# Kernel optimization log

Measured on AMD Instinct MI355X. Metric: run time of the kernel, lower is better.

## Reference

```python
import jax, jax.numpy as jnp
import numpy as np

N_NODES = 100000
N_EDGES = 1600000
N_GRAPHS = 128
D = 128          # input_dim == hidden_dim
OUT = 64         # output_dim (num classes)
L = 4            # num_layers - 1 GIN message-passing layers
BN_EPS = 1e-5


def setup_inputs() -> dict:
    key = jax.random.key(0)
    ks = jax.random.split(key, 12)
    s = 1.0 / np.sqrt(D)
    x = jax.random.normal(ks[0], (N_NODES, D), jnp.float32)
    edge_src = jax.random.randint(ks[1], (N_GRAPHS * 0 + N_EDGES,), 0, N_NODES, jnp.int32)
    edge_dst = jax.random.randint(ks[2], (N_EDGES,), 0, N_NODES, jnp.int32)
    graph_ids = jnp.sort(jax.random.randint(ks[3], (N_NODES,), 0, N_GRAPHS, jnp.int32))
    return {
        'x': x,
        'edge_src': edge_src,
        'edge_dst': edge_dst,
        'graph_ids': graph_ids,
        'eps': jnp.zeros((L,), jnp.float32),
        'W1': jax.random.normal(ks[4], (L, D, D), jnp.float32) * s,
        'b1': jnp.zeros((L, D), jnp.float32),
        'g1': jnp.ones((L, D), jnp.float32),
        'be1': jnp.zeros((L, D), jnp.float32),
        'W2': jax.random.normal(ks[5], (L, D, D), jnp.float32) * s,
        'b2': jnp.zeros((L, D), jnp.float32),
        'g2': jnp.ones((L, D), jnp.float32),
        'be2': jnp.zeros((L, D), jnp.float32),
        'predW': jax.random.normal(ks[6], (L + 1, D, OUT), jnp.float32) * s,
        'predb': jnp.zeros((L + 1, OUT), jnp.float32),
    }


def _bn(h, g, b):
    # BatchNorm1d in training mode: batch mean / biased variance over nodes
    mu = jnp.mean(h, axis=0)
    var = jnp.var(h, axis=0)
    return g * (h - mu) * jax.lax.rsqrt(var + BN_EPS) + b


def reference(x, edge_src, edge_dst, graph_ids, eps, W1, b1, g1, be1,
              W2, b2, g2, be2, predW, predb):
    n = x.shape[0]
    hidden = [x]
    h = x
    for l in range(L):
        # sparse Adj @ h : gather neighbor feats at edges, scatter-add to dst
        agg = jax.ops.segment_sum(h[edge_src], edge_dst, num_segments=n)
        pooled = agg + (1.0 + eps[l]) * h                      # GIN eps update
        z = jax.nn.relu(_bn(pooled @ W1[l] + b1[l], g1[l], be1[l]))  # MLP hidden
        z = z @ W2[l] + b2[l]                                  # MLP out
        h = jax.nn.relu(_bn(z, g2[l], be2[l]))                 # outer BN + relu
        hidden.append(h)
    # GIN readout: sum graph pooling + per-layer linear prediction (dropout p=0)
    score = jnp.zeros((N_GRAPHS, OUT), jnp.float32)
    for l, hl in enumerate(hidden):
        pooled_g = jax.ops.segment_sum(hl, graph_ids, num_segments=N_GRAPHS)
        score = score + pooled_g @ predW[l] + predb[l]
    return score
```

## Files before the change

### kernel.cpp

```cpp
#include <hip/hip_runtime.h>

#define NN 100000
#define NE 1600000
#define NG 128
#define DIM 128
#define OUTD 64
#define NL 4
#define SLCAP 48
#define NBKT 391
#define BCAP 6144
#define ECH 4096
#define EBLKS ((NE + ECH - 1) / ECH)
#define NPB 128
#define YSTR 136

typedef __attribute__((ext_vector_type(8))) short bf16x8;
typedef __attribute__((ext_vector_type(4))) float floatx4;
typedef __attribute__((ext_vector_type(2))) float floatx2;

__device__ __forceinline__ float bf_lo(unsigned u) {
    union { unsigned u; float f; } c; c.u = u << 16; return c.f;
}
__device__ __forceinline__ float bf_hi(unsigned u) {
    union { unsigned u; float f; } c; c.u = u & 0xffff0000u; return c.f;
}
__device__ __forceinline__ unsigned f2bf(float x) {
    union { float f; unsigned u; } c; c.f = x;
    return (c.u + 0x7fffu + ((c.u >> 16) & 1u)) >> 16;
}
__device__ __forceinline__ float bfs2f(short s) {
    union { unsigned u; float f; } c; c.u = ((unsigned)(unsigned short)s) << 16; return c.f;
}

__device__ __forceinline__ void bn_coef(const float* __restrict__ stat,
                                        const float* __restrict__ gamma,
                                        const float* __restrict__ beta,
                                        int f, float& a, float& c) {
    float mu = stat[f] * (1.0f / NN);
    float var = fmaf(-mu, mu, stat[DIM + f] * (1.0f / NN));
    a = gamma[f] * rsqrtf(var + 1e-5f);
    c = fmaf(-mu, a, beta[f]);
}

__global__ __launch_bounds__(256)
void bucketize(const int* __restrict__ esrc, const int* __restrict__ edst,
               int* __restrict__ gcnt, unsigned* __restrict__ bkt) {
    __shared__ int lh[NBKT];
    for (int b = threadIdx.x; b < NBKT; b += 256) lh[b] = 0;
    __syncthreads();
    const int e0 = blockIdx.x * ECH;
    const int e1 = min(e0 + ECH, NE);
    for (int e = e0 + threadIdx.x; e < e1; e += 256)
        atomicAdd(&lh[(unsigned)edst[e] >> 8], 1);
    __syncthreads();
    for (int b = threadIdx.x; b < NBKT; b += 256) {
        int c = lh[b];
        lh[b] = (c > 0) ? atomicAdd(&gcnt[b], c) : 0;
    }
    __syncthreads();
    for (int e = e0 + threadIdx.x; e < e1; e += 256) {
        unsigned d = (unsigned)edst[e];
        unsigned b = d >> 8;
        int p = atomicAdd(&lh[b], 1);
        if (p < BCAP)
            bkt[(size_t)b * BCAP + p] = (unsigned)esrc[e] | ((d & 255u) << 24);
    }
}

__global__ __launch_bounds__(256)
void bucket_to_slots(const unsigned* __restrict__ bkt, const int* __restrict__ gcnt,
                     int* __restrict__ cnt, int* __restrict__ slot) {
    __shared__ int lslot[256 * SLCAP];
    __shared__ int lc[256];
    const int b = blockIdx.x, t = threadIdx.x;
    lc[t] = 0;
    __syncthreads();
    int ne = gcnt[b]; if (ne > BCAP) ne = BCAP;
    const unsigned* be = bkt + (size_t)b * BCAP;
    for (int i = t; i < ne; i += 256) {
        unsigned v = be[i];
        int local = v >> 24;
        int pos = atomicAdd(&lc[local], 1);
        if (pos < SLCAP) lslot[local * SLCAP + pos] = (int)(v & 0xFFFFFFu);
    }
    __syncthreads();
    const int node = b * 256 + t;
    if (node < NN) cnt[node] = min(lc[t], SLCAP);
    const size_t base = (size_t)b * (256 * SLCAP);
    for (int i = t; i < 256 * SLCAP; i += 256)
        slot[base + i] = lslot[i];
}

__global__ void to_bf16(const float* __restrict__ x, unsigned* __restrict__ xb) {
    size_t i = ((size_t)blockIdx.x * 256 + threadIdx.x) * 4;
    float4 v = *(const float4*)(x + i);
    uint2 o;
    o.x = f2bf(v.x) | (f2bf(v.y) << 16);
    o.y = f2bf(v.z) | (f2bf(v.w) << 16);
    *(uint2*)(xb + i / 2) = o;
}

__global__ void build_wt(const float* __restrict__ W1, const float* __restrict__ W2,
                         unsigned short* __restrict__ Wt) {
    int b = blockIdx.x;
    const float* W = ((b & 1) ? W2 : W1) + (size_t)(b >> 1) * DIM * DIM;
    unsigned short* O = Wt + (size_t)b * DIM * DIM;
    int i = blockIdx.y * 2048 + threadIdx.x;
    for (int j = 0; j < 8; ++j, i += 256) {
        int k = i >> 7, n = i & 127;
        O[n * DIM + k] = (unsigned short)f2bf(W[i]);
    }
}

__global__ void csr_agg(const unsigned* __restrict__ hq, const int* __restrict__ cnt,
                        const int* __restrict__ slot, const float* __restrict__ eps, int l,
                        unsigned* __restrict__ outq) {
    const int t = threadIdx.x;
    const int node = blockIdx.x * 4 + (t >> 6);
    const int lane = t & 63;
    const int chunk = lane & 15;
    const int grp = lane >> 4;
    const uint4* __restrict__ h4 = (const uint4*)hq;

    const int deg = cnt[node];

    floatx2 acc[4];
    {
        uint4 sv = h4[(size_t)node * 16 + chunk];
        float e1 = (grp == 0) ? (1.0f + eps[l]) : 0.0f;
        const unsigned* p = (const unsigned*)&sv;
#pragma unroll
        for (int q = 0; q < 4; ++q) {
            floatx2 v; v.x = bf_lo(p[q]); v.y = bf_hi(p[q]);
            acc[q] = e1 * v;
        }
    }

    if (deg > 0) {
        const int iters = (deg + 15) >> 4;
        const int base = node * SLCAP;
        const int hi = base + deg - 1;
        const int j0 = base + grp;
        int idx[4];
#pragma unroll
        for (int q = 0; q < 4; ++q) {
            int j = j0 + q * 4;
            int v = slot[min(j, hi)];
            idx[q] = (j <= hi) ? v : NN;
        }

        for (int it = 0; it < iters; ++it) {
            uint4 u[4];
#pragma unroll
            for (int q = 0; q < 4; ++q) u[q] = h4[(size_t)idx[q] * 16 + chunk];

            if (it + 1 < iters) {
                const int jn = j0 + (it + 1) * 16;
#pragma unroll
                for (int q = 0; q < 4; ++q) {
                    int j = jn + q * 4;
                    int v = slot[min(j, hi)];
                    idx[q] = (j <= hi) ? v : NN;
                }
            }

#pragma unroll
            for (int q = 0; q < 4; ++q) {
                const unsigned* p = (const unsigned*)&u[q];
#pragma unroll
                for (int r = 0; r < 4; ++r) {
                    floatx2 v; v.x = bf_lo(p[r]); v.y = bf_hi(p[r]);
                    acc[r] += v;
                }
            }
        }
    }

#pragma unroll
    for (int r = 0; r < 4; ++r) {
        acc[r].x += __shfl_xor(acc[r].x, 16);
        acc[r].y += __shfl_xor(acc[r].y, 16);
        acc[r].x += __shfl_xor(acc[r].x, 32);
        acc[r].y += __shfl_xor(acc[r].y, 32);
    }
    if (grp == 0) {
        uint4 o;
        unsigned* po = (unsigned*)&o;
#pragma unroll
        for (int r = 0; r < 4; ++r)
            po[r] = f2bf(acc[r].x) | (f2bf(acc[r].y) << 16);
        ((uint4*)outq)[(size_t)node * 16 + chunk] = o;
    }
}

template<int TR>
__global__ __launch_bounds__(256, 2)
void gemm_mfma(const unsigned short* __restrict__ X, const unsigned short* __restrict__ Wt,
               const float* __restrict__ bias,
               const float* __restrict__ stat, const float* __restrict__ gamma,
               const float* __restrict__ beta,
               unsigned short* __restrict__ Y, float* __restrict__ ostat) {
    __shared__ unsigned short Ws[DIM * DIM];
    __shared__ unsigned short Ys[128 * YSTR];
    __shared__ float tatc[2 * DIM];
    float* red = (float*)Ws;
    const int t = threadIdx.x;
    const int w = t >> 6, lane = t & 63;
    const int quad = lane >> 4, m = lane & 15;
    const int rowb0 = blockIdx.x * 256 + w * 32;

#pragma unroll
    for (int i = 0; i < 8; ++i) {
        int chunk = t + i * 256;
        int r = chunk >> 4, c = chunk & 15;
        ((uint4*)Ws)[(r << 4) | (c ^ (r & 15))] = ((const uint4*)Wt)[chunk];
    }
    if (TR && t < DIM) {
        float a, c;
        bn_coef(stat, gamma, beta, t, a, c);
        tatc[t] = a; tatc[DIM + t] = c;
    }

    bf16x8 a[2][4];
#pragma unroll
    for (int rt = 0; rt < 2; ++rt) {
        int row = rowb0 + rt * 16 + m;
        if (row > NN - 1) row = NN - 1;
        const unsigned short* xr = X + (size_t)row * DIM + quad * 8;
#pragma unroll
        for (int ks = 0; ks < 4; ++ks)
            a[rt][ks] = *(const bf16x8*)(xr + ks * 32);
    }
    __syncthreads();

    float sv[8], qv[8];
#pragma unroll
    for (int ct = 0; ct < 8; ++ct) { sv[ct] = 0.f; qv[ct] = 0.f; }

    for (int sub = 0; sub < 2; ++sub) {
        if (TR) {
#pragma unroll
            for (int rt = 0; rt < 2; ++rt)
#pragma unroll
                for (int ks = 0; ks < 4; ++ks) {
                    int kk = ks * 32 + quad * 8;
                    bf16x8 v = a[rt][ks];
#pragma unroll
                    for (int j = 0; j < 8; ++j) {
                        float fv = bfs2f(v[j]);
                        fv = fmaxf(fmaf(fv, tatc[kk + j], tatc[DIM + kk + j]), 0.f);
                        v[j] = (short)f2bf(fv);
                    }
                    a[rt][ks] = v;
                }
        }

        floatx4 acc[2][8];
#pragma unroll
        for (int rt = 0; rt < 2; ++rt)
#pragma unroll
            for (int ct = 0; ct < 8; ++ct) acc[rt][ct] = (floatx4)0.f;

#pragma unroll
        for (int ct = 0; ct < 8; ++ct) {
            const int row = ct * 16 + m;
            const bf16x8* wrow = (const bf16x8*)&Ws[row * DIM];
#pragma unroll
            for (int ks = 0; ks < 4; ++ks) {
                bf16x8 b = wrow[(ks * 4 + quad) ^ m];
                acc[0][ct] = __builtin_amdgcn_mfma_f32_16x16x32_bf16(a[0][ks], b, acc[0][ct], 0, 0, 0);
                acc[1][ct] = __builtin_amdgcn_mfma_f32_16x16x32_bf16(a[1][ks], b, acc[1][ct], 0, 0, 0);
            }
        }

        if (sub == 0) {
#pragma unroll
            for (int rt = 0; rt < 2; ++rt) {
                int row = rowb0 + 128 + rt * 16 + m;
                if (row > NN - 1) row = NN - 1;
                const unsigned short* xr = X + (size_t)row * DIM + quad * 8;
#pragma unroll
                for (int ks = 0; ks < 4; ++ks)
                    a[rt][ks] = *(const bf16x8*)(xr + ks * 32);
            }
        }

#pragma unroll
        for (int ct = 0; ct < 8; ++ct) {
            int col = ct * 16 + m;
            float bv = bias[col];
            float s = 0.f, q = 0.f;
#pragma unroll
            for (int rt = 0; rt < 2; ++rt) {
#pragma unroll
                for (int r = 0; r < 4; ++r) {
                    int lrow = w * 32 + rt * 16 + quad * 4 + r;
                    int row = blockIdx.x * 256 + sub * 128 + lrow;
                    float val = acc[rt][ct][r] + bv;
                    Ys[lrow * YSTR + col] = (unsigned short)f2bf(val);
                    if (row < NN) { s += val; q = fmaf(val, val, q); }
                }
            }
            sv[ct] += s; qv[ct] += q;
        }
        __syncthreads();
        {
            int lrow = t >> 1, half = t & 1;
            int grow = blockIdx.x * 256 + sub * 128 + lrow;
            if (grow < NN) {
                const uint4* srcp = (const uint4*)&Ys[lrow * YSTR + half * 64];
                uint4* dstp = (uint4*)&Y[(size_t)grow * DIM + half * 64];
#pragma unroll
                for (int i2 = 0; i2 < 8; ++i2) dstp[i2] = srcp[i2];
            }
        }
        __syncthreads();
    }

#pragma unroll
    for (int ct = 0; ct < 8; ++ct) {
        sv[ct] += __shfl_xor(sv[ct], 16); sv[ct] += __shfl_xor(sv[ct], 32);
        qv[ct] += __shfl_xor(qv[ct], 16); qv[ct] += __shfl_xor(qv[ct], 32);
    }
    __syncthreads();
#pragma unroll
    for (int ct = 0; ct < 8; ++ct) {
        int col = ct * 16 + m;
        if (quad == 0) { red[w * 256 + col] = sv[ct]; red[w * 256 + 128 + col] = qv[ct]; }
    }
    __syncthreads();
    if (t < 256) {
        float tot = red[t] + red[256 + t] + red[512 + t] + red[768 + t];
        unsafeAtomicAdd(&ostat[t], tot);
    }
}

template<int TR>
__global__ void pool_nodes(const unsigned* __restrict__ hq, const int* __restrict__ gid,
                           const float* __restrict__ stat, const float* __restrict__ gamma,
                           const float* __restrict__ beta, float* __restrict__ pg) {
    const int lane = threadIdx.x;
    int start = blockIdx.x * NPB;
    int end = start + NPB;
    if (end > NN) end = NN;
    int f = lane * 2;
    float a0 = 0.f, c0 = 0.f, a1 = 0.f, c1 = 0.f;
    if (TR) {
        bn_coef(stat, gamma, beta, f, a0, c0);
        bn_coef(stat, gamma, beta, f + 1, a1, c1);
    }
    int cur = gid[start];
    float acc0 = 0.f, acc1 = 0.f;
    for (int i0 = start; i0 < end; i0 += 4) {
        int4 g4 = *(const int4*)(gid + i0);
        unsigned uu[4];
#pragma unroll
        for (int k = 0; k < 4; ++k) uu[k] = hq[(size_t)(i0 + k) * 64 + lane];
        int gg[4] = {g4.x, g4.y, g4.z, g4.w};
#pragma unroll
        for (int k = 0; k < 4; ++k) {
            if (gg[k] != cur) {
                unsafeAtomicAdd(&pg[cur * DIM + f], acc0);
                unsafeAtomicAdd(&pg[cur * DIM + f + 1], acc1);
                acc0 = 0.f; acc1 = 0.f;
                cur = gg[k];
            }
            float x0 = bf_lo(uu[k]), x1 = bf_hi(uu[k]);
            if (TR) {
                x0 = fmaxf(fmaf(x0, a0, c0), 0.f);
                x1 = fmaxf(fmaf(x1, a1, c1), 0.f);
            }
            acc0 += x0; acc1 += x1;
        }
    }
    unsafeAtomicAdd(&pg[cur * DIM + f], acc0);
    unsafeAtomicAdd(&pg[cur * DIM + f + 1], acc1);
}

template<int WRITE>
__global__ void norm_pool(const unsigned* __restrict__ hq, const int* __restrict__ gid,
                          const float* __restrict__ stat, const float* __restrict__ gamma,
                          const float* __restrict__ beta,
                          unsigned* __restrict__ outq, float* __restrict__ pg) {
    const int lane = threadIdx.x;
    int start = blockIdx.x * NPB;
    int end = start + NPB;
    if (end > NN) end = NN;
    int f = lane * 2;
    float a0, c0, a1, c1;
    bn_coef(stat, gamma, beta, f, a0, c0);
    bn_coef(stat, gamma, beta, f + 1, a1, c1);
    int cur = gid[start];
    float acc0 = 0.f, acc1 = 0.f;
    for (int i0 = start; i0 < end; i0 += 4) {
        int4 g4 = *(const int4*)(gid + i0);
        unsigned uu[4];
#pragma unroll
        for (int k = 0; k < 4; ++k) uu[k] = hq[(size_t)(i0 + k) * 64 + lane];
        int gg[4] = {g4.x, g4.y, g4.z, g4.w};
#pragma unroll
        for (int k = 0; k < 4; ++k) {
            if (gg[k] != cur) {
                unsafeAtomicAdd(&pg[cur * DIM + f], acc0);
                unsafeAtomicAdd(&pg[cur * DIM + f + 1], acc1);
                acc0 = 0.f; acc1 = 0.f;
                cur = gg[k];
            }
            float x0 = fmaxf(fmaf(bf_lo(uu[k]), a0, c0), 0.f);
            float x1 = fmaxf(fmaf(bf_hi(uu[k]), a1, c1), 0.f);
            if (WRITE)
                outq[(size_t)(i0 + k) * 64 + lane] = f2bf(x0) | (f2bf(x1) << 16);
            acc0 += x0; acc1 += x1;
        }
    }
    unsafeAtomicAdd(&pg[cur * DIM + f], acc0);
    unsafeAtomicAdd(&pg[cur * DIM + f + 1], acc1);
}

__global__ void final_score(const float* __restrict__ pg, const float* __restrict__ predW,
                            const float* __restrict__ predb, float* __restrict__ out) {
    int g = blockIdx.x;
    int o = threadIdx.x;
    float acc = 0.f;
    for (int l = 0; l <= NL; ++l) {
        acc += predb[l * OUTD + o];
        const float* pgr = pg + ((size_t)l * NG + g) * DIM;
        const float* w = predW + (size_t)l * DIM * OUTD;
#pragma unroll 8
        for (int k = 0; k < DIM; ++k)
            acc = fmaf(pgr[k], w[k * OUTD + o], acc);
    }
    out[g * OUTD + o] = acc;
}

extern "C" void kernel_launch(void* const* d_in, const int* in_sizes, int n_in,
                              void* d_out, int out_size, void* d_ws, size_t ws_size,
                              hipStream_t stream) {
    const float* x     = (const float*)d_in[0];
    const int*   esrc  = (const int*)d_in[1];
    const int*   edst  = (const int*)d_in[2];
    const int*   gid   = (const int*)d_in[3];
    const float* eps   = (const float*)d_in[4];
    const float* W1    = (const float*)d_in[5];
    const float* b1    = (const float*)d_in[6];
    const float* g1    = (const float*)d_in[7];
    const float* be1   = (const float*)d_in[8];
    const float* W2    = (const float*)d_in[9];
    const float* b2    = (const float*)d_in[10];
    const float* g2    = (const float*)d_in[11];
    const float* be2   = (const float*)d_in[12];
    const float* predW = (const float*)d_in[13];
    const float* predb = (const float*)d_in[14];
    float* out = (float*)d_out;

    unsigned short* XB = (unsigned short*)d_ws;
    unsigned short* A  = XB + (size_t)(NN + 1) * DIM;
    unsigned short* B  = A + (size_t)NN * DIM;
    unsigned short* WT = B + (size_t)NN * DIM;
    float* PG    = (float*)(WT + 8 * DIM * DIM);
    float* STATS = PG + 5 * NG * DIM;
    int* GCNT = (int*)(STATS + NL * 512);
    int* CNT  = GCNT + 512;
    int* SLOT = CNT + NN;
    unsigned* BKT = (unsigned*)B;

    hipMemsetAsync(PG, 0, (5 * NG * DIM + NL * 512 + 512) * sizeof(float), stream);
    hipMemsetAsync(XB + (size_t)NN * DIM, 0, DIM * sizeof(unsigned short), stream);

    bucketize<<<EBLKS, 256, 0, stream>>>(esrc, edst, GCNT, BKT);
    bucket_to_slots<<<NBKT, 256, 0, stream>>>(BKT, GCNT, CNT, SLOT);
    to_bf16<<<(NN * DIM) / 1024, 256, 0, stream>>>(x, (unsigned*)XB);
    build_wt<<<dim3(8, 8), 256, 0, stream>>>(W1, W2, WT);

    const int poolBlocks = (NN + NPB - 1) / NPB;
    const int aggBlocks  = (NN + 3) / 4;
    const int gemmBlocks = (NN + 255) / 256;

    for (int l = 0; l < NL; ++l) {
        float* STATL = STATS + l * 512;
        if (l == 0) {
            pool_nodes<0><<<poolBlocks, 64, 0, stream>>>((const unsigned*)XB, gid,
                                                         nullptr, nullptr, nullptr, PG);
        } else {
            const float* prevS = STATS + (l - 1) * 512 + 256;
            norm_pool<1><<<poolBlocks, 64, 0, stream>>>((const unsigned*)A, gid, prevS,
                                                        g2 + (l - 1) * DIM, be2 + (l - 1) * DIM,
                                                        (unsigned*)XB, PG + l * NG * DIM);
        }
        csr_agg<<<aggBlocks, 256, 0, stream>>>((const unsigned*)XB, CNT, SLOT, eps, l,
                                               (unsigned*)B);
        gemm_mfma<0><<<gemmBlocks, 256, 0, stream>>>(B, WT + (size_t)(2 * l) * DIM * DIM,
                                                     b1 + l * DIM, nullptr, nullptr, nullptr,
                                                     B, STATL);
        gemm_mfma<1><<<gemmBlocks, 256, 0, stream>>>(B, WT + (size_t)(2 * l + 1) * DIM * DIM,
                                                     b2 + l * DIM, STATL, g1 + l * DIM,
                                                     be1 + l * DIM, A, STATL + 256);
    }
    norm_pool<0><<<poolBlocks, 64, 0, stream>>>((const unsigned*)A, gid,
                                                STATS + (NL - 1) * 512 + 256,
                                                g2 + (NL - 1) * DIM, be2 + (NL - 1) * DIM,
                                                nullptr, PG + NL * NG * DIM);
    final_score<<<NG, OUTD, 0, stream>>>(PG, predW, predb, out);
}
```

Baseline: 692.8 us.

## Fuse neighbor aggregation with first MLP GEMM per layer

Replaces the separate CSR aggregation kernel and first GEMM with one kernel. Each 128-node block gathers neighbor features into shared memory, then runs the bf16 MFMA GEMM with bias and accumulates the BatchNorm statistics. This removes the round trip of the aggregated tensor through global memory and one launch per layer. In exchange each wave walks 32 nodes serially, which lowers gather parallelism and latency hiding, and shared memory use caps occupancy at two blocks per CU.

```diff
diff --git a/kernel.cpp b/kernel.cpp
--- a/kernel.cpp
+++ b/kernel.cpp
@@ -112,84 +112,172 @@
     }
 }
 
-__global__ void csr_agg(const unsigned* __restrict__ hq, const int* __restrict__ cnt,
-                        const int* __restrict__ slot, const float* __restrict__ eps, int l,
-                        unsigned* __restrict__ outq) {
+__global__ __launch_bounds__(256, 2)
+void agg_gemm(const unsigned* __restrict__ hq, const int* __restrict__ cnt,
+              const int* __restrict__ slot, const float* __restrict__ eps, int l,
+              const unsigned short* __restrict__ Wt, const float* __restrict__ bias,
+              unsigned short* __restrict__ Y, float* __restrict__ ostat) {
+    __shared__ unsigned short Ws[DIM * DIM];
+    __shared__ unsigned short Hs[128 * YSTR];
+    float* red = (float*)Ws;
     const int t = threadIdx.x;
-    const int node = blockIdx.x * 4 + (t >> 6);
-    const int lane = t & 63;
-    const int chunk = lane & 15;
-    const int grp = lane >> 4;
+    const int w = t >> 6, lane = t & 63;
+    const int quad = lane >> 4, m = lane & 15;
+    const int chunk = lane & 15, grp = lane >> 4;
     const uint4* __restrict__ h4 = (const uint4*)hq;
 
-    const int deg = cnt[node];
-
-    floatx2 acc[4];
+#pragma unroll
+    for (int i = 0; i < 8; ++i) {
+        int ch = t + i * 256;
+        int r = ch >> 4, c = ch & 15;
+        ((uint4*)Ws)[(r << 4) | (c ^ (r & 15))] = ((const uint4*)Wt)[ch];
+    }
+
+    const float e1v = 1.0f + eps[l];
+    const int nodebase = blockIdx.x * 128 + w * 32;
+    for (int nn = 0; nn < 32; ++nn) {
+        const int node = min(nodebase + nn, NN - 1);
+        const int deg = cnt[node];
+        floatx2 acc[4];
+        {
+            uint4 sv = h4[(size_t)node * 16 + chunk];
+            float e1 = (grp == 0) ? e1v : 0.0f;
+            const unsigned* p = (const unsigned*)&sv;
+#pragma unroll
+            for (int q = 0; q < 4; ++q) {
+                floatx2 v; v.x = bf_lo(p[q]); v.y = bf_hi(p[q]);
+                acc[q] = e1 * v;
+            }
+        }
+        if (deg > 0) {
+            const int iters = (deg + 15) >> 4;
+            const int base = node * SLCAP;
+            const int hi = base + deg - 1;
+            const int j0 = base + grp;
+            int idx[4];
+#pragma unroll
+            for (int q = 0; q < 4; ++q) {
+                int j = j0 + q * 4;
+                int v = slot[min(j, hi)];
+                idx[q] = (j <= hi) ? v : NN;
+            }
+            for (int it = 0; it < iters; ++it) {
+                uint4 u[4];
+#pragma unroll
+                for (int q = 0; q < 4; ++q) u[q] = h4[(size_t)idx[q] * 16 + chunk];
+                if (it + 1 < iters) {
+                    const int jn = j0 + (it + 1) * 16;
+#pragma unroll
+                    for (int q = 0; q < 4; ++q) {
+                        int j = jn + q * 4;
+                        int v = slot[min(j, hi)];
+                        idx[q] = (j <= hi) ? v : NN;
+                    }
+                }
+#pragma unroll
+                for (int q = 0; q < 4; ++q) {
+                    const unsigned* p = (const unsigned*)&u[q];
+#pragma unroll
+                    for (int r = 0; r < 4; ++r) {
+                        floatx2 v; v.x = bf_lo(p[r]); v.y = bf_hi(p[r]);
+                        acc[r] += v;
+                    }
+                }
+            }
+        }
+#pragma unroll
+        for (int r = 0; r < 4; ++r) {
+            acc[r].x += __shfl_xor(acc[r].x, 16);
+            acc[r].y += __shfl_xor(acc[r].y, 16);
+            acc[r].x += __shfl_xor(acc[r].x, 32);
+            acc[r].y += __shfl_xor(acc[r].y, 32);
+        }
+        if (grp == 0) {
+            uint4 o;
+            unsigned* po = (unsigned*)&o;
+#pragma unroll
+            for (int r = 0; r < 4; ++r)
+                po[r] = f2bf(acc[r].x) | (f2bf(acc[r].y) << 16);
+            *(uint4*)&Hs[(w * 32 + nn) * YSTR + chunk * 8] = o;
+        }
+    }
+    __syncthreads();
+
+    bf16x8 a[2][4];
+#pragma unroll
+    for (int rt = 0; rt < 2; ++rt) {
+        int lrow = w * 32 + rt * 16 + m;
+#pragma unroll
+        for (int ks = 0; ks < 4; ++ks)
+            a[rt][ks] = *(const bf16x8*)&Hs[lrow * YSTR + ks * 32 + quad * 8];
+    }
+
+    floatx4 acc[2][8];
+#pragma unroll
+    for (int rt = 0; rt < 2; ++rt)
+#pragma unroll
+        for (int ct = 0; ct < 8; ++ct) acc[rt][ct] = (floatx4)0.f;
+
+#pragma unroll
+    for (int ct = 0; ct < 8; ++ct) {
+        const int row = ct * 16 + m;
+        const bf16x8* wrow = (const bf16x8*)&Ws[row * DIM];
+#pragma unroll
+        for (int ks = 0; ks < 4; ++ks) {
+            bf16x8 b = wrow[(ks * 4 + quad) ^ m];
+            acc[0][ct] = __builtin_amdgcn_mfma_f32_16x16x32_bf16(a[0][ks], b, acc[0][ct], 0, 0, 0);
+            acc[1][ct] = __builtin_amdgcn_mfma_f32_16x16x32_bf16(a[1][ks], b, acc[1][ct], 0, 0, 0);
+        }
+    }
+    __syncthreads();
+
+    float sv[8], qv[8];
+#pragma unroll
+    for (int ct = 0; ct < 8; ++ct) { sv[ct] = 0.f; qv[ct] = 0.f; }
+#pragma unroll
+    for (int ct = 0; ct < 8; ++ct) {
+        int col = ct * 16 + m;
+        float bv = bias[col];
+        float s = 0.f, q = 0.f;
+#pragma unroll
+        for (int rt = 0; rt < 2; ++rt) {
+#pragma unroll
+            for (int r = 0; r < 4; ++r) {
+                int lrow = w * 32 + rt * 16 + quad * 4 + r;
+                int row = blockIdx.x * 128 + lrow;
+                float val = acc[rt][ct][r] + bv;
+                Hs[lrow * YSTR + col] = (unsigned short)f2bf(val);
+                if (row < NN) { s += val; q = fmaf(val, val, q); }
+            }
+        }
+        sv[ct] += s; qv[ct] += q;
+    }
+    __syncthreads();
     {
-        uint4 sv = h4[(size_t)node * 16 + chunk];
-        float e1 = (grp == 0) ? (1.0f + eps[l]) : 0.0f;
-        const unsigned* p = (const unsigned*)&sv;
-#pragma unroll
-        for (int q = 0; q < 4; ++q) {
-            floatx2 v; v.x = bf_lo(p[q]); v.y = bf_hi(p[q]);
-            acc[q] = e1 * v;
-        }
-    }
-
-    if (deg > 0) {
-        const int iters = (deg + 15) >> 4;
-        const int base = node * SLCAP;
-        const int hi = base + deg - 1;
-        const int j0 = base + grp;
-        int idx[4];
-#pragma unroll
-        for (int q = 0; q < 4; ++q) {
-            int j = j0 + q * 4;
-            int v = slot[min(j, hi)];
-            idx[q] = (j <= hi) ? v : NN;
-        }
-
-        for (int it = 0; it < iters; ++it) {
-            uint4 u[4];
-#pragma unroll
-            for (int q = 0; q < 4; ++q) u[q] = h4[(size_t)idx[q] * 16 + chunk];
-
-            if (it + 1 < iters) {
-                const int jn = j0 + (it + 1) * 16;
-#pragma unroll
-                for (int q = 0; q < 4; ++q) {
-                    int j = jn + q * 4;
-                    int v = slot[min(j, hi)];
-                    idx[q] = (j <= hi) ? v : NN;
-                }
-            }
-
-#pragma unroll
-            for (int q = 0; q < 4; ++q) {
-                const unsigned* p = (const unsigned*)&u[q];
-#pragma unroll
-                for (int r = 0; r < 4; ++r) {
-                    floatx2 v; v.x = bf_lo(p[r]); v.y = bf_hi(p[r]);
-                    acc[r] += v;
-                }
-            }
-        }
-    }
-
-#pragma unroll
-    for (int r = 0; r < 4; ++r) {
-        acc[r].x += __shfl_xor(acc[r].x, 16);
-        acc[r].y += __shfl_xor(acc[r].y, 16);
-        acc[r].x += __shfl_xor(acc[r].x, 32);
-        acc[r].y += __shfl_xor(acc[r].y, 32);
-    }
-    if (grp == 0) {
-        uint4 o;
-        unsigned* po = (unsigned*)&o;
-#pragma unroll
-        for (int r = 0; r < 4; ++r)
-            po[r] = f2bf(acc[r].x) | (f2bf(acc[r].y) << 16);
-        ((uint4*)outq)[(size_t)node * 16 + chunk] = o;
+        int lrow = t >> 1, half = t & 1;
+        int grow = blockIdx.x * 128 + lrow;
+        if (grow < NN) {
+            const uint4* srcp = (const uint4*)&Hs[lrow * YSTR + half * 64];
+            uint4* dstp = (uint4*)&Y[(size_t)grow * DIM + half * 64];
+#pragma unroll
+            for (int i2 = 0; i2 < 8; ++i2) dstp[i2] = srcp[i2];
+        }
+    }
+#pragma unroll
+    for (int ct = 0; ct < 8; ++ct) {
+        sv[ct] += __shfl_xor(sv[ct], 16); sv[ct] += __shfl_xor(sv[ct], 32);
+        qv[ct] += __shfl_xor(qv[ct], 16); qv[ct] += __shfl_xor(qv[ct], 32);
+    }
+    __syncthreads();
+#pragma unroll
+    for (int ct = 0; ct < 8; ++ct) {
+        int col = ct * 16 + m;
+        if (quad == 0) { red[w * 256 + col] = sv[ct]; red[w * 256 + 128 + col] = qv[ct]; }
+    }
+    __syncthreads();
+    if (t < 256) {
+        float tot = red[t] + red[256 + t] + red[512 + t] + red[768 + t];
+        unsafeAtomicAdd(&ostat[t], tot);
     }
 }
 
@@ -473,7 +561,7 @@
     build_wt<<<dim3(8, 8), 256, 0, stream>>>(W1, W2, WT);
 
     const int poolBlocks = (NN + NPB - 1) / NPB;
-    const int aggBlocks  = (NN + 3) / 4;
+    const int fusedBlocks = (NN + 127) / 128;
     const int gemmBlocks = (NN + 255) / 256;
 
     for (int l = 0; l < NL; ++l) {
@@ -487,11 +575,9 @@
                                                         g2 + (l - 1) * DIM, be2 + (l - 1) * DIM,
                                                         (unsigned*)XB, PG + l * NG * DIM);
         }
-        csr_agg<<<aggBlocks, 256, 0, stream>>>((const unsigned*)XB, CNT, SLOT, eps, l,
-                                               (unsigned*)B);
-        gemm_mfma<0><<<gemmBlocks, 256, 0, stream>>>(B, WT + (size_t)(2 * l) * DIM * DIM,
-                                                     b1 + l * DIM, nullptr, nullptr, nullptr,
-                                                     B, STATL);
+        agg_gemm<<<fusedBlocks, 256, 0, stream>>>((const unsigned*)XB, CNT, SLOT, eps, l,
+                                                  WT + (size_t)(2 * l) * DIM * DIM,
+                                                  b1 + l * DIM, B, STATL);
         gemm_mfma<1><<<gemmBlocks, 256, 0, stream>>>(B, WT + (size_t)(2 * l + 1) * DIM * DIM,
                                                      b2 + l * DIM, STATL, g1 + l * DIM,
                                                      be1 + l * DIM, A, STATL + 256);
```

New measurement: 875.0 us. +26.3%, slower.
